# Optimization experiments

Hardware: AMD Instinct MI355X
Metric: run time of the kernel (lower is better)

Reference implementation:

```python
import jax, jax.numpy as jnp
import numpy as np

SHAPES = [(76, 76), (38, 38), (19, 19), (1, 20)]  # 3 feature levels + task-token pseudo-level
D, HEADS, NLVL, NPTS = 256, 8, 4, 4
DH = D // HEADS
NLAYERS = 6
B = 2
S = sum(h * w for h, w in SHAPES)  # 7601


def _ref_points():
    # valid_ratios == 1 (no padding) -> normalized pixel-center grid per level, concatenated. [S,2] (x,y)
    refs = []
    for H, W in SHAPES:
        ry, rx = jnp.meshgrid(jnp.linspace(0.5, H - 0.5, H) / H,
                              jnp.linspace(0.5, W - 0.5, W) / W, indexing='ij')
        refs.append(jnp.stack([rx.ravel(), ry.ravel()], -1))
    return jnp.concatenate(refs, 0)


def _layer_norm(x, g, b):
    m = x.mean(-1, keepdims=True)
    v = ((x - m) ** 2).mean(-1, keepdims=True)
    return (x - m) * jax.lax.rsqrt(v + 1e-5) * g + b


def _bilinear(val_l, locx, locy, H, W):
    # val_l: [B, H*W, HEADS, DH]; locx/locy: [B,Q,HEADS,P] normalized coords.
    # grid_sample semantics: align_corners=False, zero padding.
    v = val_l.transpose(0, 2, 1, 3)  # [B,Hh,HW,DH]
    x = locx * W - 0.5
    y = locy * H - 0.5
    x0 = jnp.floor(x)
    y0 = jnp.floor(y)
    wx1 = x - x0
    wy1 = y - y0

    def corner(xi, yi, w):
        valid = ((xi >= 0) & (xi <= W - 1) & (yi >= 0) & (yi <= H - 1)).astype(v.dtype)
        idx = (jnp.clip(yi, 0, H - 1) * W + jnp.clip(xi, 0, W - 1)).astype(jnp.int32)
        idx_t = idx.transpose(0, 2, 1, 3)  # [B,Hh,Q,P]
        Bq, Hh, Q, P = idx_t.shape
        g = jnp.take_along_axis(v, idx_t.reshape(Bq, Hh, Q * P)[..., None], axis=2)
        g = g.reshape(Bq, Hh, Q, P, DH)
        return g * (w * valid).transpose(0, 2, 1, 3)[..., None]

    return (corner(x0, y0, (1 - wx1) * (1 - wy1)) + corner(x0 + 1, y0, wx1 * (1 - wy1))
            + corner(x0, y0 + 1, (1 - wx1) * wy1) + corner(x0 + 1, y0 + 1, wx1 * wy1))


def _msdeform(q, x, ref, Woff, boff, Wa, ba, Wv, bv, Wo, bo):
    Bq, Sq, _ = x.shape
    value = (x @ Wv + bv).reshape(Bq, Sq, HEADS, DH)
    off = (q @ Woff + boff).reshape(Bq, Sq, HEADS, NLVL, NPTS, 2)
    attn = jax.nn.softmax((q @ Wa + ba).reshape(Bq, Sq, HEADS, NLVL * NPTS), -1)
    attn = attn.reshape(Bq, Sq, HEADS, NLVL, NPTS)
    acc = jnp.zeros((Bq, HEADS, Sq, DH), x.dtype)
    start = 0
    for l, (H, W) in enumerate(SHAPES):
        n = H * W
        loc = ref[None, :, None, None, :] + off[:, :, :, l] / jnp.asarray([W, H], x.dtype)
        samp = _bilinear(value[:, start:start + n], loc[..., 0], loc[..., 1], H, W)  # [B,Hh,S,P,DH]
        a = attn[:, :, :, l].transpose(0, 2, 1, 3)  # [B,Hh,S,P]
        acc = acc + (samp * a[..., None]).sum(3)
        start += n
    return acc.transpose(0, 2, 1, 3).reshape(Bq, Sq, D) @ Wo + bo


def reference(src0, src1, src2, pos0, pos1, pos2, task_encoding, task_pos_enc, level_embed,
              W_off, b_off, W_attn, b_attn, W_val, b_val, W_out, b_out,
              W1, b1, W2, b2, g1, beta1, g2, beta2):
    srcs, poss = [src0, src1, src2], [pos0, pos1, pos2]
    sf, pf = [], []
    for l in range(3):
        Bq, C, H, W = srcs[l].shape
        sf.append(srcs[l].reshape(Bq, C, H * W).transpose(0, 2, 1))
        pf.append(poss[l].reshape(Bq, C, H * W).transpose(0, 2, 1) + level_embed[l])
    sf.append(task_encoding)
    pf.append(jnp.broadcast_to(task_pos_enc[None], task_encoding.shape))
    x = jnp.concatenate(sf, 1)   # [B,S,D]
    pos = jnp.concatenate(pf, 1)
    ref = _ref_points()
    for i in range(NLAYERS):
        q = x + pos
        x = _layer_norm(x + _msdeform(q, x, ref, W_off[i], b_off[i], W_attn[i], b_attn[i],
                                      W_val[i], b_val[i], W_out[i], b_out[i]), g1[i], beta1[i])
        x = _layer_norm(x + jax.nn.relu(x @ W1[i] + b1[i]) @ W2[i] + b2[i], g2[i], beta2[i])
    return x


def setup_inputs() -> dict:
    key = jax.random.key(0)
    ks = jax.random.split(key, 20)
    d = {}
    for i, (H, W) in enumerate(SHAPES[:3]):
        d[f'src{i}'] = jax.random.normal(ks[i], (B, D, H, W), jnp.float32)
        d[f'pos{i}'] = jax.random.normal(ks[3 + i], (B, D, H, W), jnp.float32) * 0.1
    d['task_encoding'] = jax.random.normal(ks[6], (B, 20, D), jnp.float32)
    d['task_pos_enc'] = jax.random.normal(ks[7], (20, D), jnp.float32) * 0.1
    d['level_embed'] = jax.random.normal(ks[8], (NLVL, D), jnp.float32) * 0.1

    def w(k, shape, s=0.02):
        return jax.random.normal(k, shape, jnp.float32) * s

    d['W_off'] = w(ks[9], (NLAYERS, D, HEADS * NLVL * NPTS * 2), 0.01)
    d['b_off'] = w(ks[10], (NLAYERS, HEADS * NLVL * NPTS * 2), 0.2)
    d['W_attn'] = w(ks[11], (NLAYERS, D, HEADS * NLVL * NPTS))
    d['b_attn'] = jnp.zeros((NLAYERS, HEADS * NLVL * NPTS), jnp.float32)
    d['W_val'] = w(ks[12], (NLAYERS, D, D))
    d['b_val'] = jnp.zeros((NLAYERS, D), jnp.float32)
    d['W_out'] = w(ks[13], (NLAYERS, D, D))
    d['b_out'] = jnp.zeros((NLAYERS, D), jnp.float32)
    d['W1'] = w(ks[14], (NLAYERS, D, 2048))
    d['b1'] = jnp.zeros((NLAYERS, 2048), jnp.float32)
    d['W2'] = w(ks[15], (NLAYERS, 2048, D))
    d['b2'] = jnp.zeros((NLAYERS, D), jnp.float32)
    d['g1'] = jnp.ones((NLAYERS, D), jnp.float32)
    d['beta1'] = jnp.zeros((NLAYERS, D), jnp.float32)
    d['g2'] = jnp.ones((NLAYERS, D), jnp.float32)
    d['beta2'] = jnp.zeros((NLAYERS, D), jnp.float32)
    return d
```

## Files before the change

kernel.cpp:

```cpp
#include <hip/hip_runtime.h>

#define S_TOT 7601
#define BATCH 2
#define BM (BATCH * S_TOT)
#define DMODEL 256

typedef unsigned short bf16;
typedef __attribute__((ext_vector_type(8))) short v8s;
typedef __attribute__((ext_vector_type(4))) float v4f;

__device__ __forceinline__ float b2f(bf16 u) {
    union { unsigned int i; float f; } v;
    v.i = ((unsigned int)u) << 16;
    return v.f;
}
__device__ __forceinline__ bf16 f2b(float f) {
    union { unsigned int i; float f; } v;
    v.f = f;
    unsigned int r = v.i + 0x7FFFu + ((v.i >> 16) & 1u);
    return (bf16)(r >> 16);
}
__device__ __forceinline__ float ldin(const void* p, size_t i, int isf32) {
    return isf32 ? ((const float*)p)[i] : b2f(((const bf16*)p)[i]);
}

#define GLDS16(gp, lp)                                                          \
    __builtin_amdgcn_global_load_lds(                                           \
        (const __attribute__((address_space(1))) unsigned int*)(gp),            \
        (__attribute__((address_space(3))) unsigned int*)(lp), 16, 0, 0)

__device__ __forceinline__ void xcd_remap(int& bx, int& by) {
    int gx = gridDim.x, gy = gridDim.y;
    int nwg = gx * gy;
    int lin = blockIdx.y * gx + blockIdx.x;
    int q = nwg >> 3, r = nwg & 7;
    int xcd = lin & 7, idx = lin >> 3;
    int lin2 = (xcd < r ? xcd * (q + 1) : r * (q + 1) + (xcd - r) * q) + idx;
    bx = lin2 % gx;
    by = lin2 / gx;
}

__global__ void detect_dtype(const unsigned short* __restrict__ src, int* __restrict__ flag) {
    __shared__ int cnt;
    if (threadIdx.x == 0) cnt = 0;
    __syncthreads();
    int local = 0;
    for (int i = threadIdx.x; i < 16384; i += 256) {
        unsigned int e = (src[i] >> 7) & 0xFFu;
        if (e >= 143u) local++;
    }
    atomicAdd(&cnt, local);
    __syncthreads();
    if (threadIdx.x == 0) *flag = (cnt > 200) ? 1 : 0;
}

__global__ void __launch_bounds__(256) pack_level(const void* __restrict__ src,
                                                  const void* __restrict__ pin,
                                                  const void* __restrict__ lemb, int lrow,
                                                  float* __restrict__ x,
                                                  bf16* __restrict__ pout,
                                                  int HW, int start,
                                                  const int* __restrict__ flag) {
    int isf32 = *flag;
    int i = blockIdx.x * 256 + threadIdx.x;
    int total = BATCH * HW * 256;
    if (i >= total) return;
    int c = i & 255;
    int t = i >> 8;
    int s = t % HW;
    int b = t / HW;
    size_t src_idx = ((size_t)b * 256 + c) * HW + s;
    float sv = ldin(src, src_idx, isf32);
    float pv = ldin(pin, src_idx, isf32) + ldin(lemb, (size_t)lrow * 256 + c, isf32);
    size_t o = ((size_t)b * S_TOT + start + s) * 256 + c;
    x[o] = sv;
    pout[o] = f2b(pv);
}

__global__ void __launch_bounds__(256) pack_task(const void* __restrict__ te,
                                                 const void* __restrict__ tpe,
                                                 float* __restrict__ x,
                                                 bf16* __restrict__ pout,
                                                 const int* __restrict__ flag) {
    int isf32 = *flag;
    int i = blockIdx.x * 256 + threadIdx.x;
    int total = BATCH * 20 * 256;
    if (i >= total) return;
    int c = i & 255;
    int t = (i >> 8) % 20;
    int b = (i >> 8) / 20;
    size_t o = ((size_t)b * S_TOT + 7581 + t) * 256 + c;
    x[o] = ldin(te, ((size_t)b * 20 + t) * 256 + c, isf32);
    pout[o] = f2b(ldin(tpe, (size_t)t * 256 + c, isf32));
}

__global__ void __launch_bounds__(256) make_ref(float* __restrict__ ref) {
    int s = blockIdx.x * 256 + threadIdx.x;
    if (s >= S_TOT) return;
    int H, W, st;
    if (s < 5776)      { H = 76; W = 76; st = 0; }
    else if (s < 7220) { H = 38; W = 38; st = 5776; }
    else if (s < 7581) { H = 19; W = 19; st = 7220; }
    else               { H = 1;  W = 20; st = 7581; }
    int r = s - st;
    int i = r / W, j = r % W;
    ref[s * 2 + 0] = (j + 0.5f) / (float)W;
    ref[s * 2 + 1] = (i + 0.5f) / (float)H;
}

__global__ void __launch_bounds__(256) cast_out(const float* __restrict__ x,
                                                void* __restrict__ o, int n,
                                                const int* __restrict__ flag) {
    int isf32 = *flag;
    int i = blockIdx.x * 256 + threadIdx.x;
    if (i >= n) return;
    if (isf32) ((float*)o)[i] = x[i];
    else       ((bf16*)o)[i] = f2b(x[i]);
}

__global__ void __launch_bounds__(256) cvt_x(const float* __restrict__ x,
                                             bf16* __restrict__ xb, int n4) {
    int i = blockIdx.x * 256 + threadIdx.x;
    if (i >= n4) return;
    float4 xv = ((const float4*)x)[i];
    ushort4 xo;
    xo.x = f2b(xv.x); xo.y = f2b(xv.y); xo.z = f2b(xv.z); xo.w = f2b(xv.w);
    ((ushort4*)xb)[i] = xo;
}

__global__ void __launch_bounds__(256) cvt_q(const float* __restrict__ x,
                                             const bf16* __restrict__ pos,
                                             bf16* __restrict__ qb, int n4) {
    int i = blockIdx.x * 256 + threadIdx.x;
    if (i >= n4) return;
    float4 xv = ((const float4*)x)[i];
    ushort4 pv = ((const ushort4*)pos)[i];
    ushort4 qo;
    qo.x = f2b(xv.x + b2f(pv.x));
    qo.y = f2b(xv.y + b2f(pv.y));
    qo.z = f2b(xv.z + b2f(pv.z));
    qo.w = f2b(xv.w + b2f(pv.w));
    ((ushort4*)qb)[i] = qo;
}

__global__ void __launch_bounds__(256) transpose_all(const void* __restrict__ Wv,
                                                     const void* __restrict__ Woff,
                                                     const void* __restrict__ Wa,
                                                     const void* __restrict__ Wo,
                                                     const void* __restrict__ W1,
                                                     const void* __restrict__ W2,
                                                     bf16* __restrict__ Wvt,
                                                     bf16* __restrict__ Wofft,
                                                     bf16* __restrict__ Wat,
                                                     bf16* __restrict__ Wot,
                                                     bf16* __restrict__ W1t,
                                                     bf16* __restrict__ W2t,
                                                     int L, const int* __restrict__ flag) {
    int isf32 = *flag;
    int t = blockIdx.x;
    const void* src; bf16* dst; int K, N; size_t woff;
    if (t < 64)        { src = Wv;   dst = Wvt;   K = 256;  N = 256;  woff = (size_t)L * 65536; }
    else if (t < 128)  { src = Woff; dst = Wofft; K = 256;  N = 256;  woff = (size_t)L * 65536;  t -= 64; }
    else if (t < 160)  { src = Wa;   dst = Wat;   K = 256;  N = 128;  woff = (size_t)L * 32768;  t -= 128; }
    else if (t < 224)  { src = Wo;   dst = Wot;   K = 256;  N = 256;  woff = (size_t)L * 65536;  t -= 160; }
    else if (t < 736)  { src = W1;   dst = W1t;   K = 256;  N = 2048; woff = (size_t)L * 524288; t -= 224; }
    else               { src = W2;   dst = W2t;   K = 2048; N = 256;  woff = (size_t)L * 524288; t -= 736; }
    int ntx = N >> 5;
    int tk = (t / ntx) * 32;
    int tn = (t % ntx) * 32;
    __shared__ float tl[32][33];
    int r = threadIdx.x >> 3;
    int c4 = (threadIdx.x & 7) * 4;
#pragma unroll
    for (int i = 0; i < 4; ++i)
        tl[r][c4 + i] = ldin(src, woff + (size_t)(tk + r) * N + tn + c4 + i, isf32);
    __syncthreads();
#pragma unroll
    for (int i = 0; i < 4; ++i)
        dst[(size_t)(tn + r) * K + tk + c4 + i] = f2b(tl[c4 + i][r]);
}

__global__ void __launch_bounds__(256) mfma_gemm(const bf16* __restrict__ A,
                                                 const bf16* __restrict__ Wt,
                                                 const void* __restrict__ bias, size_t boff,
                                                 bf16* __restrict__ C,
                                                 int M, int N, int K, int relu,
                                                 const int* __restrict__ flag) {
    int isf32 = *flag;
    __shared__ __align__(16) char smem[128 * 136 * 2];
    bf16* As = (bf16*)smem;
    bf16* Bs = (bf16*)smem + 8192;
    bf16* Cs = (bf16*)smem;
    int tid = threadIdx.x;
    int lane = tid & 63, wave = tid >> 6;
    int wm = (wave & 1) << 6, wn = (wave >> 1) << 6;
    int bx, by;
    xcd_remap(bx, by);
    int bm = by * 128, bn = bx * 128;
    int q = lane >> 4, l15 = lane & 15;

    v4f acc[4][4];
#pragma unroll
    for (int i = 0; i < 4; ++i)
#pragma unroll
        for (int j = 0; j < 4; ++j) acc[i][j] = (v4f){0.f, 0.f, 0.f, 0.f};

    int r0 = tid >> 2, r1 = r0 + 64;
    int oct = (tid & 3) * 8;
    int am0 = bm + r0; if (am0 >= M) am0 = M - 1;
    int am1 = bm + r1; if (am1 >= M) am1 = M - 1;
    const bf16* ag0 = A + (size_t)am0 * K + oct;
    const bf16* ag1 = A + (size_t)am1 * K + oct;
    const bf16* bg0 = Wt + (size_t)(bn + r0) * K + oct;
    const bf16* bg1 = Wt + (size_t)(bn + r1) * K + oct;
    bf16* lA0 = As + tid * 8;
    bf16* lA1 = As + (tid + 256) * 8;
    bf16* lA2 = As + 4096 + tid * 8;
    bf16* lA3 = As + 4096 + (tid + 256) * 8;
    bf16* lB0 = Bs + tid * 8;
    bf16* lB1 = Bs + (tid + 256) * 8;
    bf16* lB2 = Bs + 4096 + tid * 8;
    bf16* lB3 = Bs + 4096 + (tid + 256) * 8;

    for (int k0 = 0; k0 < K; k0 += 64) {
        GLDS16(ag0 + k0, lA0);
        GLDS16(ag1 + k0, lA1);
        GLDS16(ag0 + k0 + 32, lA2);
        GLDS16(ag1 + k0 + 32, lA3);
        GLDS16(bg0 + k0, lB0);
        GLDS16(bg1 + k0, lB1);
        GLDS16(bg0 + k0 + 32, lB2);
        GLDS16(bg1 + k0 + 32, lB3);
        __syncthreads();
#pragma unroll
        for (int h = 0; h < 2; ++h) {
            v8s a_frag[4], b_frag[4];
#pragma unroll
            for (int mi = 0; mi < 4; ++mi)
                a_frag[mi] = *(const v8s*)&As[h * 4096 + (wm + mi * 16 + l15) * 32 + q * 8];
#pragma unroll
            for (int ni = 0; ni < 4; ++ni)
                b_frag[ni] = *(const v8s*)&Bs[h * 4096 + (wn + ni * 16 + l15) * 32 + q * 8];
#pragma unroll
            for (int mi = 0; mi < 4; ++mi)
#pragma unroll
                for (int ni = 0; ni < 4; ++ni)
                    acc[mi][ni] = __builtin_amdgcn_mfma_f32_16x16x32_bf16(
                        a_frag[mi], b_frag[ni], acc[mi][ni], 0, 0, 0);
        }
        __syncthreads();
    }

#pragma unroll
    for (int ni = 0; ni < 4; ++ni) {
        int cn = wn + ni * 16 + l15;
        float bv = ldin(bias, boff + bn + cn, isf32);
#pragma unroll
        for (int mi = 0; mi < 4; ++mi) {
#pragma unroll
            for (int r = 0; r < 4; ++r) {
                float v = acc[mi][ni][r] + bv;
                if (relu) v = fmaxf(v, 0.f);
                Cs[(wm + mi * 16 + q * 4 + r) * 136 + cn] = f2b(v);
            }
        }
    }
    __syncthreads();
    {
        int row = tid >> 1, half = tid & 1;
        int gm = bm + row;
        if (gm < M) {
            const bf16* srcp = Cs + row * 136 + half * 64;
            bf16* dstp = C + (size_t)gm * N + bn + half * 64;
#pragma unroll
            for (int i = 0; i < 8; ++i)
                *(uint4*)(dstp + i * 8) = *(const uint4*)(srcp + i * 8);
        }
    }
}

__global__ void __launch_bounds__(256) mfma_gemm64(const bf16* __restrict__ A,
                                                   const bf16* __restrict__ Wt,
                                                   const void* __restrict__ bias, size_t boff,
                                                   bf16* __restrict__ C,
                                                   int M, int N, int K, int relu,
                                                   const int* __restrict__ flag) {
    int isf32 = *flag;
    __shared__ __align__(16) char smem[16384];
    bf16* As = (bf16*)smem;
    bf16* Bs = (bf16*)smem + 4096;
    bf16* Cs = (bf16*)smem;
    int tid = threadIdx.x;
    int lane = tid & 63, wave = tid >> 6;
    int wm = (wave & 1) * 32, wn = (wave >> 1) * 32;
    int bx, by;
    xcd_remap(bx, by);
    int bm = by * 64, bn = bx * 64;
    int q = lane >> 4, l15 = lane & 15;

    v4f acc[2][2];
#pragma unroll
    for (int i = 0; i < 2; ++i)
#pragma unroll
        for (int j = 0; j < 2; ++j) acc[i][j] = (v4f){0.f, 0.f, 0.f, 0.f};

    int srow = tid >> 2;
    int oct = (tid & 3) * 8;
    int am = bm + srow; if (am >= M) am = M - 1;
    const bf16* arow = A + (size_t)am * K + oct;
    const bf16* brow = Wt + (size_t)(bn + srow) * K + oct;
    bf16* lA0 = As + tid * 8;
    bf16* lA1 = As + 2048 + tid * 8;
    bf16* lB0 = Bs + tid * 8;
    bf16* lB1 = Bs + 2048 + tid * 8;

    for (int k0 = 0; k0 < K; k0 += 64) {
        GLDS16(arow + k0, lA0);
        GLDS16(arow + k0 + 32, lA1);
        GLDS16(brow + k0, lB0);
        GLDS16(brow + k0 + 32, lB1);
        __syncthreads();
#pragma unroll
        for (int h = 0; h < 2; ++h) {
            v8s a_frag[2], b_frag[2];
#pragma unroll
            for (int mi = 0; mi < 2; ++mi)
                a_frag[mi] = *(const v8s*)&As[h * 2048 + (wm + mi * 16 + l15) * 32 + q * 8];
#pragma unroll
            for (int ni = 0; ni < 2; ++ni)
                b_frag[ni] = *(const v8s*)&Bs[h * 2048 + (wn + ni * 16 + l15) * 32 + q * 8];
#pragma unroll
            for (int mi = 0; mi < 2; ++mi)
#pragma unroll
                for (int ni = 0; ni < 2; ++ni)
                    acc[mi][ni] = __builtin_amdgcn_mfma_f32_16x16x32_bf16(
                        a_frag[mi], b_frag[ni], acc[mi][ni], 0, 0, 0);
        }
        __syncthreads();
    }

#pragma unroll
    for (int ni = 0; ni < 2; ++ni) {
        int cn = wn + ni * 16 + l15;
        float bv = ldin(bias, boff + bn + cn, isf32);
#pragma unroll
        for (int mi = 0; mi < 2; ++mi) {
#pragma unroll
            for (int r = 0; r < 4; ++r) {
                float v = acc[mi][ni][r] + bv;
                if (relu) v = fmaxf(v, 0.f);
                Cs[(wm + mi * 16 + q * 4 + r) * 72 + cn] = f2b(v);
            }
        }
    }
    __syncthreads();
    {
        int row = tid >> 2, seg = tid & 3;
        int gm = bm + row;
        if (gm < M) {
            const bf16* srcp = Cs + row * 72 + seg * 16;
            bf16* dstp = C + (size_t)gm * N + bn + seg * 16;
            *(uint4*)(dstp) = *(const uint4*)(srcp);
            *(uint4*)(dstp + 8) = *(const uint4*)(srcp + 8);
        }
    }
}

template<typename TA, int ADDPOS, int RELU>
__global__ void __launch_bounds__(256) gemm_bias(const TA* __restrict__ A,
                                                 const bf16* __restrict__ Apos,
                                                 const void* __restrict__ W, size_t woff,
                                                 const void* __restrict__ bias, size_t boff,
                                                 bf16* __restrict__ C,
                                                 int M, int N, int K,
                                                 const int* __restrict__ flag) {
    int isf32 = *flag;
    __shared__ float As[16][65];
    __shared__ float Bs[16][65];
    int tid = threadIdx.x;
    int tx = tid & 15;
    int ty = tid >> 4;
    int bm = blockIdx.y * 64;
    int bn = blockIdx.x * 64;
    float acc[4][4] = {};
    for (int k0 = 0; k0 < K; k0 += 16) {
#pragma unroll
        for (int e = 0; e < 4; ++e) {
            int idx = tid + e * 256;
            int mm = idx >> 4;
            int kk = idx & 15;
            int gm = bm + mm;
            float av = 0.f;
            if (gm < M) {
                size_t ai = (size_t)gm * K + k0 + kk;
                if (sizeof(TA) == 4) av = ((const float*)A)[ai];
                else                 av = b2f(((const bf16*)A)[ai]);
                if (ADDPOS) av += b2f(Apos[ai]);
            }
            As[kk][mm] = av;
        }
#pragma unroll
        for (int e = 0; e < 4; ++e) {
            int idx = tid + e * 256;
            int kk = idx >> 6;
            int nn = idx & 63;
            int gn = bn + nn;
            Bs[kk][nn] = (gn < N) ? ldin(W, woff + (size_t)(k0 + kk) * N + gn, isf32) : 0.f;
        }
        __syncthreads();
#pragma unroll
        for (int kk = 0; kk < 16; ++kk) {
            float a[4], b[4];
#pragma unroll
            for (int i = 0; i < 4; ++i) a[i] = As[kk][ty + 16 * i];
#pragma unroll
            for (int j = 0; j < 4; ++j) b[j] = Bs[kk][tx + 16 * j];
#pragma unroll
            for (int i = 0; i < 4; ++i)
#pragma unroll
                for (int j = 0; j < 4; ++j) acc[i][j] += a[i] * b[j];
        }
        __syncthreads();
    }
#pragma unroll
    for (int i = 0; i < 4; ++i) {
        int gm = bm + ty + 16 * i;
        if (gm >= M) continue;
#pragma unroll
        for (int j = 0; j < 4; ++j) {
            int gn = bn + tx + 16 * j;
            if (gn >= N) continue;
            float v = acc[i][j] + ldin(bias, boff + gn, isf32);
            if (RELU) v = fmaxf(v, 0.f);
            C[(size_t)gm * N + gn] = f2b(v);
        }
    }
}

__global__ void __launch_bounds__(256) msdeform_sample4(const bf16* __restrict__ value,
                                                        const bf16* __restrict__ off,
                                                        const bf16* __restrict__ logits,
                                                        const float* __restrict__ refpts,
                                                        bf16* __restrict__ out) {
    __shared__ float sAttn[4 * 128];
    __shared__ int2 sIW[4 * 520];
    const int LH[4] = {76, 38, 19, 1};
    const int LW[4] = {76, 38, 19, 20};
    const int LS[4] = {0, 5776, 7220, 7581};
    int tid = threadIdx.x;
    int m0 = blockIdx.x * 4;

    for (int i = tid; i < 4 * 128; i += 256) {
        int r = i >> 7, li = i & 127;
        int m = m0 + r;
        int mc = (m < BM) ? m : BM - 1;
        sAttn[i] = b2f(logits[(size_t)mc * 128 + li]);
    }
    __syncthreads();
    if (tid < 32) {
        float* g = sAttn + tid * 16;
        float mx = -1e30f;
#pragma unroll
        for (int i = 0; i < 16; ++i) mx = fmaxf(mx, g[i]);
        float e[16], sm = 0.f;
#pragma unroll
        for (int i = 0; i < 16; ++i) { e[i] = __expf(g[i] - mx); sm += e[i]; }
        float inv = 1.f / sm;
#pragma unroll
        for (int i = 0; i < 16; ++i) g[i] = e[i] * inv;
    }
    __syncthreads();
    for (int i = tid; i < 4 * 128; i += 256) {
        int r = i >> 7, oi = i & 127;
        int m = m0 + r;
        int mc = (m < BM) ? m : BM - 1;
        int b = mc / S_TOT;
        int s = mc - b * S_TOT;
        int h = oi >> 4;
        int l = (oi >> 2) & 3;
        int H = LH[l], W = LW[l], st = LS[l];
        float fW = (float)W, fH = (float)H;
        float refx = refpts[s * 2 + 0];
        float refy = refpts[s * 2 + 1];
        ushort2 ov = *(const ushort2*)(off + (size_t)mc * 256 + oi * 2);
        float a = sAttn[r * 128 + oi];
        float xpix = (refx + b2f(ov.x) / fW) * fW - 0.5f;
        float ypix = (refy + b2f(ov.y) / fH) * fH - 0.5f;
        float x0f = floorf(xpix), y0f = floorf(ypix);
        int x0 = (int)x0f, y0 = (int)y0f;
        float wx1 = xpix - x0f, wy1 = ypix - y0f;
        float wx0 = 1.f - wx1, wy0 = 1.f - wy1;
        int vb = b * (S_TOT * 256) + h * 32;
        int base = r * 520 + h * 65 + (oi & 15) * 4;
#pragma unroll
        for (int c = 0; c < 4; ++c) {
            int cx = c & 1, cy = c >> 1;
            int xi = x0 + cx, yi = y0 + cy;
            float w = (cx ? wx1 : wx0) * (cy ? wy1 : wy0) * a;
            bool valid = (xi >= 0) && (xi <= W - 1) && (yi >= 0) && (yi <= H - 1);
            int xic = min(max(xi, 0), W - 1), yic = min(max(yi, 0), H - 1);
            int2 d;
            d.x = vb + (st + yic * W + xic) * 256;
            d.y = __float_as_int(valid ? w : 0.f);
            sIW[base + c] = d;
        }
    }
    __syncthreads();
    int r = tid >> 6, u = tid & 63;
    int h = u >> 3, d4 = (u & 7) * 4;
    int m = m0 + r;
    int cb = r * 520 + h * 65;
    float acc0 = 0.f, acc1 = 0.f, acc2 = 0.f, acc3 = 0.f;
#pragma unroll 8
    for (int c = 0; c < 64; ++c) {
        int2 p = sIW[cb + c];
        float w = __int_as_float(p.y);
        ushort4 v = *(const ushort4*)(value + p.x + d4);
        acc0 += w * b2f(v.x);
        acc1 += w * b2f(v.y);
        acc2 += w * b2f(v.z);
        acc3 += w * b2f(v.w);
    }
    if (m < BM) {
        ushort4 o;
        o.x = f2b(acc0); o.y = f2b(acc1); o.z = f2b(acc2); o.w = f2b(acc3);
        *(ushort4*)(out + (size_t)m * 256 + h * 32 + d4) = o;
    }
}

__global__ void __launch_bounds__(256) residual_ln4(float* __restrict__ x,
                                                    const bf16* __restrict__ y,
                                                    const void* __restrict__ g, size_t goff,
                                                    const void* __restrict__ beta, size_t boff,
                                                    const int* __restrict__ flag,
                                                    bf16* __restrict__ xb,
                                                    const bf16* __restrict__ pos,
                                                    bf16* __restrict__ qb) {
    int isf32 = *flag;
    int tid = threadIdx.x;
    int r = tid >> 6, lane = tid & 63;
    int m = blockIdx.x * 4 + r;
    if (m >= BM) return;
    size_t o = (size_t)m * 256 + lane * 4;
    float4 xv = *(const float4*)(x + o);
    ushort4 yv = *(const ushort4*)(y + o);
    float r0 = xv.x + b2f(yv.x), r1 = xv.y + b2f(yv.y);
    float r2 = xv.z + b2f(yv.z), r3 = xv.w + b2f(yv.w);
    float sum = r0 + r1 + r2 + r3;
#pragma unroll
    for (int ofs = 32; ofs > 0; ofs >>= 1) sum += __shfl_xor(sum, ofs);
    float mean = sum * (1.f / 256.f);
    float d0 = r0 - mean, d1 = r1 - mean, d2 = r2 - mean, d3 = r3 - mean;
    float vv = d0 * d0 + d1 * d1 + d2 * d2 + d3 * d3;
#pragma unroll
    for (int ofs = 32; ofs > 0; ofs >>= 1) vv += __shfl_xor(vv, ofs);
    float rstd = rsqrtf(vv * (1.f / 256.f) + 1e-5f);
    int c = lane * 4;
    float o0 = d0 * rstd * ldin(g, goff + c + 0, isf32) + ldin(beta, boff + c + 0, isf32);
    float o1 = d1 * rstd * ldin(g, goff + c + 1, isf32) + ldin(beta, boff + c + 1, isf32);
    float o2 = d2 * rstd * ldin(g, goff + c + 2, isf32) + ldin(beta, boff + c + 2, isf32);
    float o3 = d3 * rstd * ldin(g, goff + c + 3, isf32) + ldin(beta, boff + c + 3, isf32);
    *(float4*)(x + o) = make_float4(o0, o1, o2, o3);
    if (xb) {
        ushort4 xo;
        xo.x = f2b(o0); xo.y = f2b(o1); xo.z = f2b(o2); xo.w = f2b(o3);
        *(ushort4*)(xb + o) = xo;
    }
    if (qb) {
        ushort4 pv = *(const ushort4*)(pos + o);
        ushort4 qo;
        qo.x = f2b(o0 + b2f(pv.x));
        qo.y = f2b(o1 + b2f(pv.y));
        qo.z = f2b(o2 + b2f(pv.z));
        qo.w = f2b(o3 + b2f(pv.w));
        *(ushort4*)(qb + o) = qo;
    }
}

extern "C" void kernel_launch(void* const* d_in, const int* in_sizes, int n_in,
                              void* d_out, int out_size, void* d_ws, size_t ws_size,
                              hipStream_t stream) {
    (void)in_sizes; (void)n_in; (void)out_size;
    const size_t MS = (size_t)BM * DMODEL;

    char* base = (char*)d_ws;
    int* flag    = (int*)base;    base += 256;
    float* x     = (float*)base;  base += MS * 4;
    bf16* value  = (bf16*)base;   base += MS * 2;
    bf16* attnl  = (bf16*)base;   base += (size_t)BM * 128 * 2;
    bf16* pos    = (bf16*)base;   base += MS * 2;
    bf16* offms  = (bf16*)base;   base += MS * 2;
    bf16* yb     = (bf16*)base;   base += MS * 2;
    size_t base_used = (size_t)(base - (char*)d_ws);

    bf16* xb = (bf16*)base;
    size_t need_fast = base_used + MS * 2
                     + (size_t)2048 * 256 * 2 * 2
                     + (size_t)256 * 256 * 2 * 3
                     + (size_t)128 * 256 * 2
                     + (size_t)S_TOT * 2 * 4 + 1024;
    bool FAST = ws_size >= need_fast;

    bf16 *W1t = nullptr, *W2t = nullptr, *Wvt = nullptr, *Wofft = nullptr, *Wot = nullptr, *Wat = nullptr;
    float* ref;
    bf16* hiddenF = nullptr;
    bool FULLH = false;
    if (FAST) {
        char* p = (char*)xb + MS * 2;
        W1t = (bf16*)p;   p += (size_t)2048 * 256 * 2;
        W2t = (bf16*)p;   p += (size_t)2048 * 256 * 2;
        Wvt = (bf16*)p;   p += (size_t)256 * 256 * 2;
        Wofft = (bf16*)p; p += (size_t)256 * 256 * 2;
        Wot = (bf16*)p;   p += (size_t)256 * 256 * 2;
        Wat = (bf16*)p;   p += (size_t)128 * 256 * 2;
        ref = (float*)p;  p += (size_t)S_TOT * 2 * 4;
        size_t used = (size_t)(p - (char*)d_ws);
        used = (used + 255) & ~(size_t)255;
        if (ws_size >= used + (size_t)BM * 2048 * 2) {
            hiddenF = (bf16*)((char*)d_ws + used);
            FULLH = true;
        }
    } else {
        ref = (float*)base;
    }

    bf16* hidden = FULLH ? hiddenF : value;
    const int CH = FULLH ? BM : 2816;

    detect_dtype<<<1, 256, 0, stream>>>((const unsigned short*)d_in[0], flag);

    {
        int HW0 = 76 * 76, HW1 = 38 * 38, HW2 = 19 * 19;
        int n0 = BATCH * HW0 * 256, n1 = BATCH * HW1 * 256, n2 = BATCH * HW2 * 256;
        pack_level<<<(n0 + 255) / 256, 256, 0, stream>>>(d_in[0], d_in[1], d_in[8], 0, x, pos, HW0, 0, flag);
        pack_level<<<(n1 + 255) / 256, 256, 0, stream>>>(d_in[2], d_in[3], d_in[8], 1, x, pos, HW1, 5776, flag);
        pack_level<<<(n2 + 255) / 256, 256, 0, stream>>>(d_in[4], d_in[5], d_in[8], 2, x, pos, HW2, 7220, flag);
        int nt = BATCH * 20 * 256;
        pack_task<<<(nt + 255) / 256, 256, 0, stream>>>(d_in[6], d_in[7], x, pos, flag);
        make_ref<<<(S_TOT + 255) / 256, 256, 0, stream>>>(ref);
    }

    const int GM64 = (BM + 63) / 64;
    const int GR4 = (BM + 3) / 4;
    const int n4 = (int)(MS / 4);

    if (FAST) {
        cvt_x<<<(n4 + 255) / 256, 256, 0, stream>>>(x, xb, n4);
        cvt_q<<<(n4 + 255) / 256, 256, 0, stream>>>(x, pos, yb, n4);
    }

    for (int L = 0; L < 6; ++L) {
        size_t oW256 = (size_t)L * 256 * 256, ob256 = (size_t)L * 256;
        size_t oW128 = (size_t)L * 256 * 128, ob128 = (size_t)L * 128;
        size_t oW1   = (size_t)L * 256 * 2048, ob1  = (size_t)L * 2048;
        size_t oW2   = (size_t)L * 2048 * 256;

        if (FAST) {
            transpose_all<<<1248, 256, 0, stream>>>(d_in[13], d_in[9], d_in[11], d_in[15], d_in[17], d_in[19],
                                                    Wvt, Wofft, Wat, Wot, W1t, W2t, L, flag);
            bf16* qb = yb;
            mfma_gemm64<<<dim3(4, GM64), 256, 0, stream>>>(xb, Wvt, d_in[14], ob256, value, BM, 256, 256, 0, flag);
            mfma_gemm64<<<dim3(4, GM64), 256, 0, stream>>>(qb, Wofft, d_in[10], ob256, offms, BM, 256, 256, 0, flag);
            mfma_gemm64<<<dim3(2, GM64), 256, 0, stream>>>(qb, Wat, d_in[12], ob128, attnl, BM, 128, 256, 0, flag);

            msdeform_sample4<<<GR4, 256, 0, stream>>>(value, offms, attnl, ref, offms);

            mfma_gemm64<<<dim3(4, GM64), 256, 0, stream>>>(offms, Wot, d_in[16], ob256, yb, BM, 256, 256, 0, flag);
            residual_ln4<<<GR4, 256, 0, stream>>>(x, yb, d_in[21], ob256, d_in[22], ob256, flag, xb, nullptr, nullptr);

            for (int r0 = 0; r0 < BM; r0 += CH) {
                int mc = BM - r0 < CH ? BM - r0 : CH;
                int gmc128 = (mc + 127) / 128;
                int gmc64 = (mc + 63) / 64;
                mfma_gemm<<<dim3(16, gmc128), 256, 0, stream>>>(xb + (size_t)r0 * 256, W1t, d_in[18], ob1,
                                                                hidden, mc, 2048, 256, 1, flag);
                mfma_gemm64<<<dim3(4, gmc64), 256, 0, stream>>>(hidden, W2t, d_in[20], ob256,
                                                                yb + (size_t)r0 * 256, mc, 256, 2048, 0, flag);
            }
            residual_ln4<<<GR4, 256, 0, stream>>>(x, yb, d_in[23], ob256, d_in[24], ob256, flag, xb,
                                                  (L < 5) ? pos : nullptr, (L < 5) ? yb : nullptr);
        } else {
            dim3 g256(4, GM64);
            dim3 g128(2, GM64);
            gemm_bias<float, 0, 0><<<g256, 256, 0, stream>>>(x, nullptr, d_in[13], oW256, d_in[14], ob256,
                                                             value, BM, 256, 256, flag);
            gemm_bias<float, 1, 0><<<g256, 256, 0, stream>>>(x, pos, d_in[9], oW256, d_in[10], ob256,
                                                             offms, BM, 256, 256, flag);
            gemm_bias<float, 1, 0><<<g128, 256, 0, stream>>>(x, pos, d_in[11], oW128, d_in[12], ob128,
                                                             attnl, BM, 128, 256, flag);
            msdeform_sample4<<<GR4, 256, 0, stream>>>(value, offms, attnl, ref, offms);
            gemm_bias<bf16, 0, 0><<<g256, 256, 0, stream>>>(offms, nullptr, d_in[15], oW256, d_in[16], ob256,
                                                            yb, BM, 256, 256, flag);
            residual_ln4<<<GR4, 256, 0, stream>>>(x, yb, d_in[21], ob256, d_in[22], ob256, flag, nullptr, nullptr, nullptr);
            for (int r0 = 0; r0 < BM; r0 += CH) {
                int mc = BM - r0 < CH ? BM - r0 : CH;
                dim3 gh(32, (mc + 63) / 64);
                dim3 go(4, (mc + 63) / 64);
                gemm_bias<float, 0, 1><<<gh, 256, 0, stream>>>(x + (size_t)r0 * 256, nullptr, d_in[17], oW1,
                                                               d_in[18], ob1, hidden, mc, 2048, 256, flag);
                gemm_bias<bf16, 0, 0><<<go, 256, 0, stream>>>(hidden, nullptr, d_in[19], oW2, d_in[20], ob256,
                                                              yb + (size_t)r0 * 256, mc, 256, 2048, flag);
            }
            residual_ln4<<<GR4, 256, 0, stream>>>(x, yb, d_in[23], ob256, d_in[24], ob256, flag, nullptr, nullptr, nullptr);
        }
    }

    cast_out<<<((int)MS + 255) / 256, 256, 0, stream>>>(x, d_out, (int)MS, flag);
}
```

Measured before the change: 1.258 ms.

## Fuse offset/attention GEMMs, merge casts, and transpose all layer weights upfront

Merges the offset and attention-logit projections into one GEMM over a concatenated 384-wide transposed weight, so the query activation is read once per layer. It also merges the x and q cast kernels into one pass, and transposes weights for all six layers in a single launch when the workspace is large enough. This cuts per-layer launches and redundant activation reads, at the cost of more workspace. When the workspace is too small it falls back to transposing one layer at a time.

```diff
diff --git a/kernel.cpp b/kernel.cpp
--- a/kernel.cpp
+++ b/kernel.cpp
@@ -118,28 +118,21 @@
     else       ((bf16*)o)[i] = f2b(x[i]);
 }
 
-__global__ void __launch_bounds__(256) cvt_x(const float* __restrict__ x,
-                                             bf16* __restrict__ xb, int n4) {
-    int i = blockIdx.x * 256 + threadIdx.x;
-    if (i >= n4) return;
-    float4 xv = ((const float4*)x)[i];
-    ushort4 xo;
-    xo.x = f2b(xv.x); xo.y = f2b(xv.y); xo.z = f2b(xv.z); xo.w = f2b(xv.w);
-    ((ushort4*)xb)[i] = xo;
-}
-
-__global__ void __launch_bounds__(256) cvt_q(const float* __restrict__ x,
-                                             const bf16* __restrict__ pos,
-                                             bf16* __restrict__ qb, int n4) {
+__global__ void __launch_bounds__(256) cvt_xq(const float* __restrict__ x,
+                                              const bf16* __restrict__ pos,
+                                              bf16* __restrict__ xb,
+                                              bf16* __restrict__ qb, int n4) {
     int i = blockIdx.x * 256 + threadIdx.x;
     if (i >= n4) return;
     float4 xv = ((const float4*)x)[i];
     ushort4 pv = ((const ushort4*)pos)[i];
-    ushort4 qo;
+    ushort4 xo, qo;
+    xo.x = f2b(xv.x); xo.y = f2b(xv.y); xo.z = f2b(xv.z); xo.w = f2b(xv.w);
     qo.x = f2b(xv.x + b2f(pv.x));
     qo.y = f2b(xv.y + b2f(pv.y));
     qo.z = f2b(xv.z + b2f(pv.z));
     qo.w = f2b(xv.w + b2f(pv.w));
+    ((ushort4*)xb)[i] = xo;
     ((ushort4*)qb)[i] = qo;
 }
 
@@ -150,21 +143,22 @@
                                                      const void* __restrict__ W1,
                                                      const void* __restrict__ W2,
                                                      bf16* __restrict__ Wvt,
-                                                     bf16* __restrict__ Wofft,
-                                                     bf16* __restrict__ Wat,
+                                                     bf16* __restrict__ Wqt,
                                                      bf16* __restrict__ Wot,
                                                      bf16* __restrict__ W1t,
                                                      bf16* __restrict__ W2t,
-                                                     int L, const int* __restrict__ flag) {
+                                                     int L0, const int* __restrict__ flag) {
     int isf32 = *flag;
+    int L = (L0 >= 0) ? L0 : (int)blockIdx.y;
+    size_t dl = (L0 >= 0) ? 0 : (size_t)blockIdx.y;
     int t = blockIdx.x;
-    const void* src; bf16* dst; int K, N; size_t woff;
-    if (t < 64)        { src = Wv;   dst = Wvt;   K = 256;  N = 256;  woff = (size_t)L * 65536; }
-    else if (t < 128)  { src = Woff; dst = Wofft; K = 256;  N = 256;  woff = (size_t)L * 65536;  t -= 64; }
-    else if (t < 160)  { src = Wa;   dst = Wat;   K = 256;  N = 128;  woff = (size_t)L * 32768;  t -= 128; }
-    else if (t < 224)  { src = Wo;   dst = Wot;   K = 256;  N = 256;  woff = (size_t)L * 65536;  t -= 160; }
-    else if (t < 736)  { src = W1;   dst = W1t;   K = 256;  N = 2048; woff = (size_t)L * 524288; t -= 224; }
-    else               { src = W2;   dst = W2t;   K = 2048; N = 256;  woff = (size_t)L * 524288; t -= 736; }
+    const void* src; bf16* dst; int K, N; size_t woff; int rowoff = 0;
+    if (t < 64)        { src = Wv;   dst = Wvt + dl * 65536;  K = 256;  N = 256;  woff = (size_t)L * 65536; }
+    else if (t < 128)  { src = Woff; dst = Wqt + dl * 98304;  K = 256;  N = 256;  woff = (size_t)L * 65536;  t -= 64; }
+    else if (t < 160)  { src = Wa;   dst = Wqt + dl * 98304;  K = 256;  N = 128;  woff = (size_t)L * 32768;  rowoff = 256; t -= 128; }
+    else if (t < 224)  { src = Wo;   dst = Wot + dl * 65536;  K = 256;  N = 256;  woff = (size_t)L * 65536;  t -= 160; }
+    else if (t < 736)  { src = W1;   dst = W1t + dl * 524288; K = 256;  N = 2048; woff = (size_t)L * 524288; t -= 224; }
+    else               { src = W2;   dst = W2t + dl * 524288; K = 2048; N = 256;  woff = (size_t)L * 524288; t -= 736; }
     int ntx = N >> 5;
     int tk = (t / ntx) * 32;
     int tn = (t % ntx) * 32;
@@ -177,7 +171,7 @@
     __syncthreads();
 #pragma unroll
     for (int i = 0; i < 4; ++i)
-        dst[(size_t)(tn + r) * K + tk + c4 + i] = f2b(tl[c4 + i][r]);
+        dst[(size_t)(tn + r + rowoff) * K + tk + c4 + i] = f2b(tl[c4 + i][r]);
 }
 
 __global__ void __launch_bounds__(256) mfma_gemm(const bf16* __restrict__ A,
@@ -360,6 +354,100 @@
         if (gm < M) {
             const bf16* srcp = Cs + row * 72 + seg * 16;
             bf16* dstp = C + (size_t)gm * N + bn + seg * 16;
+            *(uint4*)(dstp) = *(const uint4*)(srcp);
+            *(uint4*)(dstp + 8) = *(const uint4*)(srcp + 8);
+        }
+    }
+}
+
+__global__ void __launch_bounds__(256) mfma_gemm64_q(const bf16* __restrict__ A,
+                                                     const bf16* __restrict__ Wt,
+                                                     const void* __restrict__ bias0, size_t boff0,
+                                                     const void* __restrict__ bias1, size_t boff1,
+                                                     bf16* __restrict__ out0,
+                                                     bf16* __restrict__ out1,
+                                                     int M, int K,
+                                                     const int* __restrict__ flag) {
+    int isf32 = *flag;
+    __shared__ __align__(16) char smem[16384];
+    bf16* As = (bf16*)smem;
+    bf16* Bs = (bf16*)smem + 4096;
+    bf16* Cs = (bf16*)smem;
+    int tid = threadIdx.x;
+    int lane = tid & 63, wave = tid >> 6;
+    int wm = (wave & 1) * 32, wn = (wave >> 1) * 32;
+    int bx, by;
+    xcd_remap(bx, by);
+    int bm = by * 64, bn = bx * 64;
+    int q = lane >> 4, l15 = lane & 15;
+
+    v4f acc[2][2];
+#pragma unroll
+    for (int i = 0; i < 2; ++i)
+#pragma unroll
+        for (int j = 0; j < 2; ++j) acc[i][j] = (v4f){0.f, 0.f, 0.f, 0.f};
+
+    int srow = tid >> 2;
+    int oct = (tid & 3) * 8;
+    int am = bm + srow; if (am >= M) am = M - 1;
+    const bf16* arow = A + (size_t)am * K + oct;
+    const bf16* brow = Wt + (size_t)(bn + srow) * K + oct;
+    bf16* lA0 = As + tid * 8;
+    bf16* lA1 = As + 2048 + tid * 8;
+    bf16* lB0 = Bs + tid * 8;
+    bf16* lB1 = Bs + 2048 + tid * 8;
+
+    for (int k0 = 0; k0 < K; k0 += 64) {
+        GLDS16(arow + k0, lA0);
+        GLDS16(arow + k0 + 32, lA1);
+        GLDS16(brow + k0, lB0);
+        GLDS16(brow + k0 + 32, lB1);
+        __syncthreads();
+#pragma unroll
+        for (int h = 0; h < 2; ++h) {
+            v8s a_frag[2], b_frag[2];
+#pragma unroll
+            for (int mi = 0; mi < 2; ++mi)
+                a_frag[mi] = *(const v8s*)&As[h * 2048 + (wm + mi * 16 + l15) * 32 + q * 8];
+#pragma unroll
+            for (int ni = 0; ni < 2; ++ni)
+                b_frag[ni] = *(const v8s*)&Bs[h * 2048 + (wn + ni * 16 + l15) * 32 + q * 8];
+#pragma unroll
+            for (int mi = 0; mi < 2; ++mi)
+#pragma unroll
+                for (int ni = 0; ni < 2; ++ni)
+                    acc[mi][ni] = __builtin_amdgcn_mfma_f32_16x16x32_bf16(
+                        a_frag[mi], b_frag[ni], acc[mi][ni], 0, 0, 0);
+        }
+        __syncthreads();
+    }
+
+    int isOff = (bn < 256);
+    bf16* outp = isOff ? out0 : out1;
+    int outN = isOff ? 256 : 128;
+    int colbase = isOff ? bn : bn - 256;
+    const void* bptr = isOff ? bias0 : bias1;
+    size_t bofs = isOff ? boff0 : boff1;
+
+#pragma unroll
+    for (int ni = 0; ni < 2; ++ni) {
+        int cn = wn + ni * 16 + l15;
+        float bv = ldin(bptr, bofs + colbase + cn, isf32);
+#pragma unroll
+        for (int mi = 0; mi < 2; ++mi) {
+#pragma unroll
+            for (int r = 0; r < 4; ++r) {
+                Cs[(wm + mi * 16 + q * 4 + r) * 72 + cn] = f2b(acc[mi][ni][r] + bv);
+            }
+        }
+    }
+    __syncthreads();
+    {
+        int row = tid >> 2, seg = tid & 3;
+        int gm = bm + row;
+        if (gm < M) {
+            const bf16* srcp = Cs + row * 72 + seg * 16;
+            bf16* dstp = outp + (size_t)gm * outN + colbase + seg * 16;
             *(uint4*)(dstp) = *(const uint4*)(srcp);
             *(uint4*)(dstp + 8) = *(const uint4*)(srcp + 8);
         }
@@ -593,27 +681,30 @@
     bf16* yb     = (bf16*)base;   base += MS * 2;
     size_t base_used = (size_t)(base - (char*)d_ws);
 
+    const size_t SZ_WVT = 65536, SZ_WQT = 98304, SZ_WOT = 65536, SZ_W1T = 524288, SZ_W2T = 524288;
+    const size_t WB1 = (SZ_WVT + SZ_WQT + SZ_WOT + SZ_W1T + SZ_W2T) * 2;
+
     bf16* xb = (bf16*)base;
-    size_t need_fast = base_used + MS * 2
-                     + (size_t)2048 * 256 * 2 * 2
-                     + (size_t)256 * 256 * 2 * 3
-                     + (size_t)128 * 256 * 2
-                     + (size_t)S_TOT * 2 * 4 + 1024;
-    bool FAST = ws_size >= need_fast;
-
-    bf16 *W1t = nullptr, *W2t = nullptr, *Wvt = nullptr, *Wofft = nullptr, *Wot = nullptr, *Wat = nullptr;
+    size_t needB  = base_used + MS * 2 + WB1 + (size_t)S_TOT * 8 + 1024;
+    size_t needBH = ((needB + 255) & ~(size_t)255) + (size_t)BM * 2048 * 2;
+    size_t needAH = ((base_used + MS * 2 + 6 * WB1 + (size_t)S_TOT * 8 + 1024 + 255) & ~(size_t)255)
+                  + (size_t)BM * 2048 * 2;
+    bool FAST = ws_size >= needB;
+    bool W6   = ws_size >= needAH;
+    int  nL   = W6 ? 6 : 1;
+
+    bf16 *W1t = nullptr, *W2t = nullptr, *Wvt = nullptr, *Wqt = nullptr, *Wot = nullptr;
     float* ref;
     bf16* hiddenF = nullptr;
     bool FULLH = false;
     if (FAST) {
         char* p = (char*)xb + MS * 2;
-        W1t = (bf16*)p;   p += (size_t)2048 * 256 * 2;
-        W2t = (bf16*)p;   p += (size_t)2048 * 256 * 2;
-        Wvt = (bf16*)p;   p += (size_t)256 * 256 * 2;
-        Wofft = (bf16*)p; p += (size_t)256 * 256 * 2;
-        Wot = (bf16*)p;   p += (size_t)256 * 256 * 2;
-        Wat = (bf16*)p;   p += (size_t)128 * 256 * 2;
-        ref = (float*)p;  p += (size_t)S_TOT * 2 * 4;
+        Wvt = (bf16*)p;  p += (size_t)nL * SZ_WVT * 2;
+        Wqt = (bf16*)p;  p += (size_t)nL * SZ_WQT * 2;
+        Wot = (bf16*)p;  p += (size_t)nL * SZ_WOT * 2;
+        W1t = (bf16*)p;  p += (size_t)nL * SZ_W1T * 2;
+        W2t = (bf16*)p;  p += (size_t)nL * SZ_W2T * 2;
+        ref = (float*)p; p += (size_t)S_TOT * 2 * 4;
         size_t used = (size_t)(p - (char*)d_ws);
         used = (used + 255) & ~(size_t)255;
         if (ws_size >= used + (size_t)BM * 2048 * 2) {
@@ -645,8 +736,12 @@
     const int n4 = (int)(MS / 4);
 
     if (FAST) {
-        cvt_x<<<(n4 + 255) / 256, 256, 0, stream>>>(x, xb, n4);
-        cvt_q<<<(n4 + 255) / 256, 256, 0, stream>>>(x, pos, yb, n4);
+        cvt_xq<<<(n4 + 255) / 256, 256, 0, stream>>>(x, pos, xb, yb, n4);
+        if (W6) {
+            transpose_all<<<dim3(1248, 6), 256, 0, stream>>>(d_in[13], d_in[9], d_in[11], d_in[15],
+                                                             d_in[17], d_in[19],
+                                                             Wvt, Wqt, Wot, W1t, W2t, -1, flag);
+        }
     }
 
     for (int L = 0; L < 6; ++L) {
@@ -656,25 +751,33 @@
         size_t oW2   = (size_t)L * 2048 * 256;
 
         if (FAST) {
-            transpose_all<<<1248, 256, 0, stream>>>(d_in[13], d_in[9], d_in[11], d_in[15], d_in[17], d_in[19],
-                                                    Wvt, Wofft, Wat, Wot, W1t, W2t, L, flag);
+            bf16* WvtL = Wvt + (W6 ? (size_t)L * SZ_WVT : 0);
+            bf16* WqtL = Wqt + (W6 ? (size_t)L * SZ_WQT : 0);
+            bf16* WotL = Wot + (W6 ? (size_t)L * SZ_WOT : 0);
+            bf16* W1tL = W1t + (W6 ? (size_t)L * SZ_W1T : 0);
+            bf16* W2tL = W2t + (W6 ? (size_t)L * SZ_W2T : 0);
+            if (!W6) {
+                transpose_all<<<dim3(1248, 1), 256, 0, stream>>>(d_in[13], d_in[9], d_in[11], d_in[15],
+                                                                 d_in[17], d_in[19],
+                                                                 Wvt, Wqt, Wot, W1t, W2t, L, flag);
+            }
             bf16* qb = yb;
-            mfma_gemm64<<<dim3(4, GM64), 256, 0, stream>>>(xb, Wvt, d_in[14], ob256, value, BM, 256, 256, 0, flag);
-            mfma_gemm64<<<dim3(4, GM64), 256, 0, stream>>>(qb, Wofft, d_in[10], ob256, offms, BM, 256, 256, 0, flag);
-            mfma_gemm64<<<dim3(2, GM64), 256, 0, stream>>>(qb, Wat, d_in[12], ob128, attnl, BM, 128, 256, 0, flag);
+            mfma_gemm64<<<dim3(4, GM64), 256, 0, stream>>>(xb, WvtL, d_in[14], ob256, value, BM, 256, 256, 0, flag);
+            mfma_gemm64_q<<<dim3(6, GM64), 256, 0, stream>>>(qb, WqtL, d_in[10], ob256, d_in[12], ob128,
+                                                             offms, attnl, BM, 256, flag);
 
             msdeform_sample4<<<GR4, 256, 0, stream>>>(value, offms, attnl, ref, offms);
 
-            mfma_gemm64<<<dim3(4, GM64), 256, 0, stream>>>(offms, Wot, d_in[16], ob256, yb, BM, 256, 256, 0, flag);
+            mfma_gemm64<<<dim3(4, GM64), 256, 0, stream>>>(offms, WotL, d_in[16], ob256, yb, BM, 256, 256, 0, flag);
             residual_ln4<<<GR4, 256, 0, stream>>>(x, yb, d_in[21], ob256, d_in[22], ob256, flag, xb, nullptr, nullptr);
 
             for (int r0 = 0; r0 < BM; r0 += CH) {
                 int mc = BM - r0 < CH ? BM - r0 : CH;
                 int gmc128 = (mc + 127) / 128;
                 int gmc64 = (mc + 63) / 64;
-                mfma_gemm<<<dim3(16, gmc128), 256, 0, stream>>>(xb + (size_t)r0 * 256, W1t, d_in[18], ob1,
+                mfma_gemm<<<dim3(16, gmc128), 256, 0, stream>>>(xb + (size_t)r0 * 256, W1tL, d_in[18], ob1,
                                                                 hidden, mc, 2048, 256, 1, flag);
-                mfma_gemm64<<<dim3(4, gmc64), 256, 0, stream>>>(hidden, W2t, d_in[20], ob256,
+                mfma_gemm64<<<dim3(4, gmc64), 256, 0, stream>>>(hidden, W2tL, d_in[20], ob256,
                                                                 yb + (size_t)r0 * 256, mc, 256, 2048, 0, flag);
             }
             residual_ln4<<<GR4, 256, 0, stream>>>(x, yb, d_in[23], ob256, d_in[24], ob256, flag, xb,
```

Measured after the change: 1.202 ms. -4.5%, faster.
